# Kernel tuning notes

Measured on AMD Instinct MI355X. Metric: run time of the kernel, lower is better.

Reference implementation:

```python
import jax, jax.numpy as jnp
from jax import lax
import numpy as np

B, S, V, E, H, W = 32, 1024, 32000, 512, 512, 128  # batch, seq, vocab, emb, hidden, n_word_segments


def setup_inputs() -> dict:
    key = jax.random.key(0)
    ks = jax.random.split(key, 12)
    bound = 1.0 / np.sqrt(H)  # torch GRU default init: U(-1/sqrt(H), 1/sqrt(H))
    u = lambda k, shape: jax.random.uniform(k, shape, jnp.float32, -bound, bound)
    step = S // W
    inp = {
        "input_seqs": jax.random.randint(ks[0], (B, S), 0, V, dtype=jnp.int32),
        "input_lens": jnp.full((B,), S, dtype=jnp.int32),  # full lengths -> pack/pad is identity
        "hidden": jnp.zeros((2, B, H), jnp.float32),  # torch code ignores the passed hidden
        "layout": jnp.broadcast_to(jnp.arange(W + 1, dtype=jnp.int32) * step, (B, W + 1)),
        "emb": jax.random.normal(ks[1], (V, E), jnp.float32),
        "W_ih_f": u(ks[2], (3 * H, E)),
        "W_hh_f": u(ks[3], (3 * H, H)),
        "b_ih_f": u(ks[4], (3 * H,)),
        "b_hh_f": u(ks[5], (3 * H,)),
        "W_ih_b": u(ks[6], (3 * H, E)),
        "W_hh_b": u(ks[7], (3 * H, H)),
        "b_ih_b": u(ks[8], (3 * H,)),
        "b_hh_b": u(ks[9], (3 * H,)),
    }
    return inp


def _gru_dir(x, W_ih, W_hh, b_ih, b_hh, reverse):
    # x: [B,S,E]. Precompute input gates once (big GEMM), then scan the recurrence.
    gx = jnp.einsum('bse,ge->sbg', x, W_ih) + b_ih  # [S,B,3H], time-major
    h0 = jnp.zeros((x.shape[0], H), x.dtype)

    def step(h, g):
        gh = h @ W_hh.T + b_hh  # [B,3H]
        r = jax.nn.sigmoid(g[:, :H] + gh[:, :H])
        z = jax.nn.sigmoid(g[:, H:2 * H] + gh[:, H:2 * H])
        n = jnp.tanh(g[:, 2 * H:] + r * gh[:, 2 * H:])
        hn = (1.0 - z) * n + z * h
        return hn, hn

    hT, ys = lax.scan(step, h0, gx, reverse=reverse)  # ys: [S,B,H] aligned to original time order
    return ys.transpose(1, 0, 2), hT


def _segment_max(outputs, layout):
    # outputs: [B,S,2H]; layout: [B,W+1] sorted boundaries, layout[:,0]=0, layout[:,-1]=S.
    t = jnp.arange(S)
    seg = jax.vmap(lambda lay: jnp.searchsorted(lay, t, side='right') - 1)(layout)  # [B,S]
    gid = (jnp.arange(B)[:, None] * W + seg).reshape(-1)  # [B*S]
    flat = outputs.reshape(B * S, -1)
    mx = jax.ops.segment_max(flat, gid, num_segments=B * W)
    cnt = jax.ops.segment_sum(jnp.ones((B * S,), flat.dtype), gid, num_segments=B * W)
    mx = jnp.where(cnt[:, None] > 0, mx, 0.0)  # zero-pad empty segments (matches torch padding)
    return mx.reshape(B, W, -1)


def reference(input_seqs, input_lens, hidden, layout,
              emb, W_ih_f, W_hh_f, b_ih_f, b_hh_f, W_ih_b, W_hh_b, b_ih_b, b_hh_b):
    emb0 = emb.at[0].set(0.0)  # padding_idx=0
    x = emb0[input_seqs]  # [B,S,E]
    out_f, h_f = _gru_dir(x, W_ih_f, W_hh_f, b_ih_f, b_hh_f, reverse=False)
    out_b, h_b = _gru_dir(x, W_ih_b, W_hh_b, b_ih_b, b_hh_b, reverse=True)
    outputs = jnp.concatenate([out_f, out_b], axis=-1)  # [B,S,2H]
    hidden_out = jnp.stack([h_f, h_b], axis=0)  # [2,B,H]
    maxed = _segment_max(outputs, layout)  # [B,W,2H]
    return maxed, hidden_out
```

## Files before the change

### kernel.cpp

```cpp
#include <hip/hip_runtime.h>
#include <hip/hip_bf16.h>

#define Bb 32
#define Ss 1024
#define Vv 32000
#define Ee 512
#define Hh 512
#define Ww 128
#define GXC 3072
#define MR  (Bb * Ss)

typedef short short8  __attribute__((ext_vector_type(8)));
typedef float floatx4 __attribute__((ext_vector_type(4)));
typedef _Float16 f16x2 __attribute__((ext_vector_type(2)));
typedef unsigned long long u64;

__device__ inline float dot2f(unsigned w, unsigned h, float acc) {
  return __builtin_amdgcn_fdot2(__builtin_bit_cast(f16x2, w),
                                __builtin_bit_cast(f16x2, h), acc, false);
}
__device__ inline unsigned short bf16bits(float x) {
  return __builtin_bit_cast(unsigned short, __float2bfloat16(x));
}

template<typename T> __device__ inline T gxstore(float v);
template<> __device__ inline float gxstore<float>(float v) { return v; }
template<> __device__ inline __hip_bfloat16 gxstore<__hip_bfloat16>(float v) { return __float2bfloat16(v); }
template<typename T> __device__ inline float gxload(T v);
template<> __device__ inline float gxload<float>(float v) { return v; }
template<> __device__ inline float gxload<__hip_bfloat16>(__hip_bfloat16 v) { return __bfloat162float(v); }


__global__ void prep_emb(const float* __restrict__ emb, unsigned short* __restrict__ out) {
  int i = (blockIdx.x * 256 + threadIdx.x) * 4;
  float4 v = *reinterpret_cast<const float4*>(emb + i);
  bool z = (i < Ee);
  ushort4 o;
  o.x = z ? (unsigned short)0 : bf16bits(v.x);
  o.y = z ? (unsigned short)0 : bf16bits(v.y);
  o.z = z ? (unsigned short)0 : bf16bits(v.z);
  o.w = z ? (unsigned short)0 : bf16bits(v.w);
  *reinterpret_cast<ushort4*>(out + i) = o;
}

__global__ void prep_wih(const float* __restrict__ wf, const float* __restrict__ wb,
                         unsigned short* __restrict__ out) {
  int i = (blockIdx.x * 256 + threadIdx.x) * 4;
  const float* src = (i < 1536 * 512) ? (wf + i) : (wb + (i - 1536 * 512));
  float4 v = *reinterpret_cast<const float4*>(src);
  ushort4 o;
  o.x = bf16bits(v.x); o.y = bf16bits(v.y); o.z = bf16bits(v.z); o.w = bf16bits(v.w);
  *reinterpret_cast<ushort4*>(out + i) = o;
}

__global__ void prep_whh(const float* __restrict__ wf, const float* __restrict__ wb,
                         unsigned* __restrict__ out) {
  int o = blockIdx.x * 256 + threadIdx.x;
  int m    = o & 3;
  int u4   = o >> 2;
  int tid  = u4 & 511;
  int rest = u4 >> 9;
  int i    = rest & 15;
  int rest2 = rest >> 4;
  int g    = rest2 % 3;
  int rest3 = rest2 / 3;
  int j    = rest3 & 3;
  int dir  = rest3 >> 2;
  int c    = tid >> 2;
  int q    = tid & 3;
  int row  = g * 512 + j * 128 + c;
  int kp   = q * 64 + i * 4 + m;
  const float* W = dir ? wb : wf;
  unsigned lo = __builtin_bit_cast(unsigned short, (_Float16)W[(size_t)row * Hh + 2 * kp]);
  unsigned hi = __builtin_bit_cast(unsigned short, (_Float16)W[(size_t)row * Hh + 2 * kp + 1]);
  out[o] = lo | (hi << 16);
}

__global__ void zero_hx(unsigned* __restrict__ hxw) {
  hxw[blockIdx.x * 256 + threadIdx.x] = 0u;
}

template<typename GXT>
__global__ __launch_bounds__(256)
void gx_gemm(const int* __restrict__ seq, const unsigned short* __restrict__ embb,
             const unsigned short* __restrict__ wihb, GXT* __restrict__ gx) {
  __shared__ short As[128][80];
  __shared__ short Bs[128][80];
  __shared__ int toks[128];
  const int tid = threadIdx.x;
  const int m0 = blockIdx.y * 128;
  const int n0 = blockIdx.x * 128;
  if (tid < 128) {
    int r = m0 + tid;
    toks[tid] = seq[(r & 31) * Ss + (r >> 5)];
  }
  __syncthreads();
  const int lane = tid & 63, wave = tid >> 6;
  const int wm = (wave >> 1) * 64, wn = (wave & 1) * 64;
  floatx4 zero = {0.f, 0.f, 0.f, 0.f};
  floatx4 acc[4][4];
  #pragma unroll
  for (int a = 0; a < 4; ++a)
    #pragma unroll
    for (int c = 0; c < 4; ++c) acc[a][c] = zero;

  for (int k0 = 0; k0 < Ee; k0 += 64) {
    #pragma unroll
    for (int i = 0; i < 4; ++i) {
      int slot = i * 256 + tid;
      int row = slot >> 3, cq = (slot & 7) * 8;
      uint4 va = *reinterpret_cast<const uint4*>(embb + (size_t)toks[row] * Ee + k0 + cq);
      *reinterpret_cast<uint4*>(&As[row][cq]) = va;
      uint4 vb = *reinterpret_cast<const uint4*>(wihb + (size_t)(n0 + row) * Ee + k0 + cq);
      *reinterpret_cast<uint4*>(&Bs[row][cq]) = vb;
    }
    __syncthreads();
    #pragma unroll
    for (int ks = 0; ks < 2; ++ks) {
      short8 af[4], bfr[4];
      #pragma unroll
      for (int mi = 0; mi < 4; ++mi)
        af[mi] = *reinterpret_cast<const short8*>(&As[wm + mi * 16 + (lane & 15)][ks * 32 + (lane >> 4) * 8]);
      #pragma unroll
      for (int ni = 0; ni < 4; ++ni)
        bfr[ni] = *reinterpret_cast<const short8*>(&Bs[wn + ni * 16 + (lane & 15)][ks * 32 + (lane >> 4) * 8]);
      #pragma unroll
      for (int mi = 0; mi < 4; ++mi)
        #pragma unroll
        for (int ni = 0; ni < 4; ++ni)
          acc[mi][ni] = __builtin_amdgcn_mfma_f32_16x16x32_bf16(af[mi], bfr[ni], acc[mi][ni], 0, 0, 0);
    }
    __syncthreads();
  }
  #pragma unroll
  for (int mi = 0; mi < 4; ++mi) {
    #pragma unroll
    for (int ni = 0; ni < 4; ++ni) {
      int r0 = m0 + wm + mi * 16 + ((lane >> 4) * 4);
      int c  = n0 + wn + ni * 16 + (lane & 15);
      #pragma unroll
      for (int j = 0; j < 4; ++j)
        gx[(size_t)(r0 + j) * GXC + c] = gxstore<GXT>(acc[mi][ni][j]);
    }
  }
}


#define H16(M) M(0) M(1) M(2) M(3) M(4) M(5) M(6) M(7) \
               M(8) M(9) M(10) M(11) M(12) M(13) M(14) M(15)

#define WDECL(i) uint4 W0_##i, W1_##i, W2_##i;
#define WLOAD(i) W0_##i = wq[(i) * 512]; \
                 W1_##i = wq[(16 + (i)) * 512]; \
                 W2_##i = wq[(32 + (i)) * 512];
#define WPIN(i) asm volatile("" : "+v"(W0_##i.x), "+v"(W0_##i.y), "+v"(W0_##i.z), "+v"(W0_##i.w), \
                                  "+v"(W1_##i.x), "+v"(W1_##i.y), "+v"(W1_##i.z), "+v"(W1_##i.w), \
                                  "+v"(W2_##i.x), "+v"(W2_##i.y), "+v"(W2_##i.z), "+v"(W2_##i.w));
#define CHUNK(i) { uint4 Hq = hq4[i]; \
  s0 = dot2f(W0_##i.x, Hq.x, s0); s0 = dot2f(W0_##i.y, Hq.y, s0); \
  s0 = dot2f(W0_##i.z, Hq.z, s0); s0 = dot2f(W0_##i.w, Hq.w, s0); \
  s1 = dot2f(W1_##i.x, Hq.x, s1); s1 = dot2f(W1_##i.y, Hq.y, s1); \
  s1 = dot2f(W1_##i.z, Hq.z, s1); s1 = dot2f(W1_##i.w, Hq.w, s1); \
  s2 = dot2f(W2_##i.x, Hq.x, s2); s2 = dot2f(W2_##i.y, Hq.y, s2); \
  s2 = dot2f(W2_##i.z, Hq.z, s2); s2 = dot2f(W2_##i.w, Hq.w, s2); }

#define TAGOK1(a, want) \
  (((((unsigned)((a) >> 16)) & 0xffffu) == (want)) & \
   ((((unsigned)((a) >> 48))) == (want)))

template<typename GXT>
__global__ __launch_bounds__(512, 2)
void rnn_kernel(const GXT* __restrict__ gx, const unsigned* __restrict__ whh2,
                const float* __restrict__ bih_f, const float* __restrict__ bhh_f,
                const float* __restrict__ bih_b, const float* __restrict__ bhh_b,
                const int* __restrict__ layout, float* __restrict__ out,
                unsigned* __restrict__ hx) {
  __shared__ unsigned hbufw[544];
  __shared__ int lay[Ww + 1];
  const int tid   = threadIdx.x;
  const int j     = blockIdx.x >> 6;
  const int chain = blockIdx.x & 63;
  const int dir   = chain >> 5;
  const int b     = chain & 31;
  const int c     = tid >> 2;
  const int q     = tid & 3;
  const int col   = j * 128 + c;

  const uint4* wq = reinterpret_cast<const uint4*>(whh2)
                    + (size_t)(dir * 4 + j) * 48 * 512 + tid;
  H16(WDECL)
  H16(WLOAD)
  H16(WPIN)

  float bi0 = 0.f, bi1 = 0.f, bi2 = 0.f, bh0 = 0.f, bh1 = 0.f, bh2 = 0.f;
  if (q == 0) {
    const float* bi = dir ? bih_b : bih_f;
    const float* bh = dir ? bhh_b : bhh_f;
    bi0 = bi[col]; bi1 = bi[512 + col]; bi2 = bi[1024 + col];
    bh0 = bh[col]; bh1 = bh[512 + col]; bh2 = bh[1024 + col];
  }
  if (tid <= Ww) lay[tid] = layout[b * (Ww + 1) + tid];
  hbufw[tid] = 0u;
  if (tid < 32) hbufw[512 + tid] = 0u;
  __syncthreads();

  float h = 0.f, mx = -3.0e38f;
  int t = dir ? (Ss - 1) : 0;
  const int tstep = dir ? -1 : 1;
  int seg = dir ? (Ww - 1) : 0;
  int p = 0;

  float gr = 0.f, gz = 0.f, gn = 0.f;
  if (q == 0) {
    const GXT* gp = gx + (size_t)(t * Bb + b) * GXC + dir * 1536 + col;
    gr = gxload<GXT>(gp[0]); gz = gxload<GXT>(gp[512]); gn = gxload<GXT>(gp[1024]);
  }

  #pragma unroll 1
  for (int it = 0; it < Ss; ++it, t += tstep) {
    float ngr = 0.f, ngz = 0.f, ngn = 0.f;
    if (q == 0 && it + 1 < Ss) {
      const GXT* gp = gx + (size_t)((t + tstep) * Bb + b) * GXC + dir * 1536 + col;
      ngr = gxload<GXT>(gp[0]); ngz = gxload<GXT>(gp[512]); ngn = gxload<GXT>(gp[1024]);
    }
    float s0 = 0.f, s1 = 0.f, s2 = 0.f;
    const uint4* hq4 = reinterpret_cast<const uint4*>(hbufw) + p * 68 + q * 17;
    H16(CHUNK)
    H16(WPIN)
    { float u;
      u = __shfl_xor(s0, 1); s0 += u; u = __shfl_xor(s0, 2); s0 += u;
      u = __shfl_xor(s1, 1); s1 += u; u = __shfl_xor(s1, 2); s1 += u;
      u = __shfl_xor(s2, 1); s2 += u; u = __shfl_xor(s2, 2); s2 += u; }
    const int P = p ^ 1;
    if (q == 0) {
      float rs = gr + bi0 + bh0 + s0;
      float zs = gz + bi1 + bh1 + s1;
      float nh = bh2 + s2;
      float r = 1.f / (1.f + __expf(-rs));
      float z = 1.f / (1.f + __expf(-zs));
      float x = gn + bi2 + r * nh;
      x = fminf(fmaxf(x, -15.f), 15.f);
      float e = __expf(2.f * x);
      float n = (e - 1.f) / (e + 1.f);
      h = (1.f - z) * n + z * h;
      unsigned hb16 = (unsigned)__builtin_bit_cast(unsigned short, (_Float16)h);
      __hip_atomic_store(hx + ((((size_t)P * 64 + chain) * 4 + j) << 7) + c,
                         (((unsigned)(it + 1)) << 16) | hb16,
                         __ATOMIC_RELAXED, __HIP_MEMORY_SCOPE_AGENT);
      mx = fmaxf(mx, h);
      reinterpret_cast<_Float16*>(hbufw)[((P * 272 + j * 68 + (c >> 1)) << 1) | (c & 1)]
          = (_Float16)h;
      bool flush = dir ? (t == lay[seg]) : (t + 1 == lay[seg + 1]);
      if (flush) {
        out[(size_t)(b * Ww + seg) * 1024 + dir * 512 + col] = mx;
        mx = -3.0e38f;
        seg += tstep;
      }
    }
    if (it + 1 < Ss && tid < 192) {
      int s = tid >> 6, qd = tid & 63;
      int sib = s + (s >= j);
      const u64* src = reinterpret_cast<const u64*>(
          hx + ((((size_t)P * 64 + chain) * 4 + sib) << 7) + (qd << 1));
      const unsigned want = (unsigned)(it + 1);
      u64 a;
      for (;;) {
        a = __hip_atomic_load(src, __ATOMIC_RELAXED, __HIP_MEMORY_SCOPE_AGENT);
        if (TAGOK1(a, want)) break;
      }
      hbufw[P * 272 + sib * 68 + qd] =
          ((unsigned)a & 0xffffu) | (((unsigned)(a >> 32) & 0xffffu) << 16);
    }
    __syncthreads();
    p = P;
    gr = ngr; gz = ngz; gn = ngn;
  }
  if (q == 0)
    out[(size_t)Bb * Ww * 1024 + (size_t)dir * (Bb * Hh) + b * Hh + col] = h;
}

extern "C" void kernel_launch(void* const* d_in, const int* in_sizes, int n_in,
                              void* d_out, int out_size, void* d_ws, size_t ws_size,
                              hipStream_t stream) {
  const int*   seq    = (const int*)  d_in[0];
  const int*   layout = (const int*)  d_in[3];
  const float* emb    = (const float*)d_in[4];
  const float* Wih_f  = (const float*)d_in[5];
  const float* Whh_f  = (const float*)d_in[6];
  const float* bih_f  = (const float*)d_in[7];
  const float* bhh_f  = (const float*)d_in[8];
  const float* Wih_b  = (const float*)d_in[9];
  const float* Whh_b  = (const float*)d_in[10];
  const float* bih_b  = (const float*)d_in[11];
  const float* bhh_b  = (const float*)d_in[12];
  float* out = (float*)d_out;

  char* ws = (char*)d_ws;
  unsigned short* embb  = (unsigned short*)ws;
  unsigned short* wihb  = (unsigned short*)(ws + 32768000);
  unsigned*       whh2  = (unsigned*)      (ws + 35913728);
  unsigned*       hxw   = (unsigned*)      (ws + 39059456);
  void*           gxp   = (void*)          (ws + 39321600);

  const size_t need_f32 = 39321600ULL + (size_t)MR * GXC * 4;
  const size_t need_b16 = 39321600ULL + (size_t)MR * GXC * 2;
  if (ws_size < need_b16) return;

  prep_emb<<<(Vv * Ee) / 4 / 256, 256, 0, stream>>>(emb, embb);
  prep_wih<<<(GXC * Ee) / 4 / 256, 256, 0, stream>>>(Wih_f, Wih_b, wihb);
  prep_whh<<<(2 * 4 * 48 * 512 * 4) / 256, 256, 0, stream>>>(Whh_f, Whh_b, whh2);
  zero_hx<<<256, 256, 0, stream>>>(hxw);

  if (ws_size >= need_f32) {
    gx_gemm<float><<<dim3(GXC / 128, MR / 128), 256, 0, stream>>>(seq, embb, wihb, (float*)gxp);
    rnn_kernel<float><<<256, 512, 0, stream>>>((const float*)gxp, whh2,
                                               bih_f, bhh_f, bih_b, bhh_b, layout, out, hxw);
  } else {
    gx_gemm<__hip_bfloat16><<<dim3(GXC / 128, MR / 128), 256, 0, stream>>>(seq, embb, wihb, (__hip_bfloat16*)gxp);
    rnn_kernel<__hip_bfloat16><<<256, 512, 0, stream>>>((const __hip_bfloat16*)gxp, whh2,
                                                        bih_f, bhh_f, bih_b, bhh_b, layout, out, hxw);
  }
}
```

Baseline: 2.492 ms.

## Use MFMA 16x16x32 f16 for recurrent matvec with AGPR-resident weights

Replaces the per-thread fdot2 recurrent matvec with MFMA instructions. The hidden vector is fed as the A operand, so only one of the 16 rows is useful, and the W_hh slices stay pinned in accumulator registers. The W_hh prepack layout is reworked to match the MFMA B-operand layout. Gate sums go through a shared buffer, which adds an extra __syncthreads per timestep. The per-step latency is traded against wasting fifteen-sixteenths of the MFMA work and adding a barrier.

```diff
diff --git a/kernel.cpp b/kernel.cpp
--- a/kernel.cpp
+++ b/kernel.cpp
@@ -12,15 +12,14 @@
 
 typedef short short8  __attribute__((ext_vector_type(8)));
 typedef float floatx4 __attribute__((ext_vector_type(4)));
-typedef _Float16 f16x2 __attribute__((ext_vector_type(2)));
+typedef _Float16 f16x8 __attribute__((ext_vector_type(8)));
 typedef unsigned long long u64;
 
-__device__ inline float dot2f(unsigned w, unsigned h, float acc) {
-  return __builtin_amdgcn_fdot2(__builtin_bit_cast(f16x2, w),
-                                __builtin_bit_cast(f16x2, h), acc, false);
-}
 __device__ inline unsigned short bf16bits(float x) {
   return __builtin_bit_cast(unsigned short, __float2bfloat16(x));
+}
+__device__ inline unsigned f16w(float x) {
+  return (unsigned)__builtin_bit_cast(unsigned short, (_Float16)x);
 }
 
 template<typename T> __device__ inline T gxstore(float v);
@@ -56,24 +55,24 @@
 __global__ void prep_whh(const float* __restrict__ wf, const float* __restrict__ wb,
                          unsigned* __restrict__ out) {
   int o = blockIdx.x * 256 + threadIdx.x;
-  int m    = o & 3;
+  int d    = o & 3;
   int u4   = o >> 2;
-  int tid  = u4 & 511;
-  int rest = u4 >> 9;
-  int i    = rest & 15;
-  int rest2 = rest >> 4;
-  int g    = rest2 % 3;
-  int rest3 = rest2 / 3;
-  int j    = rest3 & 3;
-  int dir  = rest3 >> 2;
-  int c    = tid >> 2;
-  int q    = tid & 3;
-  int row  = g * 512 + j * 128 + c;
-  int kp   = q * 64 + i * 4 + m;
+  int l    = u4 & 63;
+  int kt   = (u4 >> 6) & 15;
+  int rest = u4 >> 10;
+  int s    = rest % 3;
+  int wj   = rest / 3;
+  int w    = wj & 7;
+  int dj   = wj >> 3;
+  int j    = dj & 3;
+  int dir  = dj >> 2;
+  int pair = w * 3 + s;
+  int g    = pair >> 3;
+  int n    = pair & 7;
+  int row  = g * 512 + j * 128 + n * 16 + (l & 15);
+  int k    = kt * 32 + ((l >> 4) << 3) + 2 * d;
   const float* W = dir ? wb : wf;
-  unsigned lo = __builtin_bit_cast(unsigned short, (_Float16)W[(size_t)row * Hh + 2 * kp]);
-  unsigned hi = __builtin_bit_cast(unsigned short, (_Float16)W[(size_t)row * Hh + 2 * kp + 1]);
-  out[o] = lo | (hi << 16);
+  out[o] = f16w(W[(size_t)row * Hh + k]) | (f16w(W[(size_t)row * Hh + k + 1]) << 16);
 }
 
 __global__ void zero_hx(unsigned* __restrict__ hxw) {
@@ -150,19 +149,20 @@
                M(8) M(9) M(10) M(11) M(12) M(13) M(14) M(15)
 
 #define WDECL(i) uint4 W0_##i, W1_##i, W2_##i;
-#define WLOAD(i) W0_##i = wq[(i) * 512]; \
-                 W1_##i = wq[(16 + (i)) * 512]; \
-                 W2_##i = wq[(32 + (i)) * 512];
-#define WPIN(i) asm volatile("" : "+v"(W0_##i.x), "+v"(W0_##i.y), "+v"(W0_##i.z), "+v"(W0_##i.w), \
-                                  "+v"(W1_##i.x), "+v"(W1_##i.y), "+v"(W1_##i.z), "+v"(W1_##i.w), \
-                                  "+v"(W2_##i.x), "+v"(W2_##i.y), "+v"(W2_##i.z), "+v"(W2_##i.w));
-#define CHUNK(i) { uint4 Hq = hq4[i]; \
-  s0 = dot2f(W0_##i.x, Hq.x, s0); s0 = dot2f(W0_##i.y, Hq.y, s0); \
-  s0 = dot2f(W0_##i.z, Hq.z, s0); s0 = dot2f(W0_##i.w, Hq.w, s0); \
-  s1 = dot2f(W1_##i.x, Hq.x, s1); s1 = dot2f(W1_##i.y, Hq.y, s1); \
-  s1 = dot2f(W1_##i.z, Hq.z, s1); s1 = dot2f(W1_##i.w, Hq.w, s1); \
-  s2 = dot2f(W2_##i.x, Hq.x, s2); s2 = dot2f(W2_##i.y, Hq.y, s2); \
-  s2 = dot2f(W2_##i.z, Hq.z, s2); s2 = dot2f(W2_##i.w, Hq.w, s2); }
+#define WLOAD(i) W0_##i = wq[(i) * 64]; \
+                 W1_##i = wq[(16 + (i)) * 64]; \
+                 W2_##i = wq[(32 + (i)) * 64];
+#define WPINA(i) asm volatile("" : "+a"(W0_##i.x), "+a"(W0_##i.y), "+a"(W0_##i.z), "+a"(W0_##i.w), \
+                                   "+a"(W1_##i.x), "+a"(W1_##i.y), "+a"(W1_##i.z), "+a"(W1_##i.w), \
+                                   "+a"(W2_##i.x), "+a"(W2_##i.y), "+a"(W2_##i.z), "+a"(W2_##i.w));
+#define CHUNKM(i) { \
+  short8 ar = *reinterpret_cast<const short8*>(hbytes + pb + ((i) << 6) + aoff); \
+  acc0 = __builtin_amdgcn_mfma_f32_16x16x32_f16(__builtin_bit_cast(f16x8, ar), \
+         __builtin_bit_cast(f16x8, W0_##i), acc0, 0, 0, 0); \
+  acc1 = __builtin_amdgcn_mfma_f32_16x16x32_f16(__builtin_bit_cast(f16x8, ar), \
+         __builtin_bit_cast(f16x8, W1_##i), acc1, 0, 0, 0); \
+  acc2 = __builtin_amdgcn_mfma_f32_16x16x32_f16(__builtin_bit_cast(f16x8, ar), \
+         __builtin_bit_cast(f16x8, W2_##i), acc2, 0, 0, 0); }
 
 #define TAGOK1(a, want) \
   (((((unsigned)((a) >> 16)) & 0xffffu) == (want)) & \
@@ -175,33 +175,35 @@
                 const float* __restrict__ bih_b, const float* __restrict__ bhh_b,
                 const int* __restrict__ layout, float* __restrict__ out,
                 unsigned* __restrict__ hx) {
-  __shared__ unsigned hbufw[544];
+  __shared__ unsigned hbufw[512];
+  __shared__ float sbuf[3][128];
   __shared__ int lay[Ww + 1];
   const int tid   = threadIdx.x;
+  const int w     = tid >> 6;
+  const int lane  = tid & 63;
   const int j     = blockIdx.x >> 6;
   const int chain = blockIdx.x & 63;
   const int dir   = chain >> 5;
   const int b     = chain & 31;
-  const int c     = tid >> 2;
-  const int q     = tid & 3;
-  const int col   = j * 128 + c;
 
   const uint4* wq = reinterpret_cast<const uint4*>(whh2)
-                    + (size_t)(dir * 4 + j) * 48 * 512 + tid;
+                    + (size_t)((dir * 4 + j) * 8 + w) * 3072 + lane;
   H16(WDECL)
   H16(WLOAD)
-  H16(WPIN)
-
-  float bi0 = 0.f, bi1 = 0.f, bi2 = 0.f, bh0 = 0.f, bh1 = 0.f, bh2 = 0.f;
-  if (q == 0) {
+  H16(WPINA)
+
+  float br0 = 0.f, bz0 = 0.f, bi2 = 0.f, bh2 = 0.f;
+  if (tid < 128) {
     const float* bi = dir ? bih_b : bih_f;
-    const float* bh = dir ? bhh_b : bhh_f;
-    bi0 = bi[col]; bi1 = bi[512 + col]; bi2 = bi[1024 + col];
-    bh0 = bh[col]; bh1 = bh[512 + col]; bh2 = bh[1024 + col];
+    const float* bv = dir ? bhh_b : bhh_f;
+    int col = j * 128 + tid;
+    br0 = bi[col] + bv[col];
+    bz0 = bi[512 + col] + bv[512 + col];
+    bi2 = bi[1024 + col];
+    bh2 = bv[1024 + col];
   }
   if (tid <= Ww) lay[tid] = layout[b * (Ww + 1) + tid];
   hbufw[tid] = 0u;
-  if (tid < 32) hbufw[512 + tid] = 0u;
   __syncthreads();
 
   float h = 0.f, mx = -3.0e38f;
@@ -209,33 +211,39 @@
   const int tstep = dir ? -1 : 1;
   int seg = dir ? (Ww - 1) : 0;
   int p = 0;
+  const char* hbytes = reinterpret_cast<const char*>(hbufw);
+  const int aoff = (lane >> 4) << 4;
 
   float gr = 0.f, gz = 0.f, gn = 0.f;
-  if (q == 0) {
-    const GXT* gp = gx + (size_t)(t * Bb + b) * GXC + dir * 1536 + col;
+  if (tid < 128) {
+    const GXT* gp = gx + (size_t)(t * Bb + b) * GXC + dir * 1536 + j * 128 + tid;
     gr = gxload<GXT>(gp[0]); gz = gxload<GXT>(gp[512]); gn = gxload<GXT>(gp[1024]);
   }
 
   #pragma unroll 1
   for (int it = 0; it < Ss; ++it, t += tstep) {
     float ngr = 0.f, ngz = 0.f, ngn = 0.f;
-    if (q == 0 && it + 1 < Ss) {
-      const GXT* gp = gx + (size_t)((t + tstep) * Bb + b) * GXC + dir * 1536 + col;
+    if (tid < 128 && it + 1 < Ss) {
+      const GXT* gp = gx + (size_t)((t + tstep) * Bb + b) * GXC + dir * 1536 + j * 128 + tid;
       ngr = gxload<GXT>(gp[0]); ngz = gxload<GXT>(gp[512]); ngn = gxload<GXT>(gp[1024]);
     }
-    float s0 = 0.f, s1 = 0.f, s2 = 0.f;
-    const uint4* hq4 = reinterpret_cast<const uint4*>(hbufw) + p * 68 + q * 17;
-    H16(CHUNK)
-    H16(WPIN)
-    { float u;
-      u = __shfl_xor(s0, 1); s0 += u; u = __shfl_xor(s0, 2); s0 += u;
-      u = __shfl_xor(s1, 1); s1 += u; u = __shfl_xor(s1, 2); s1 += u;
-      u = __shfl_xor(s2, 1); s2 += u; u = __shfl_xor(s2, 2); s2 += u; }
+    floatx4 acc0 = {0.f, 0.f, 0.f, 0.f};
+    floatx4 acc1 = acc0, acc2 = acc0;
+    const int pb = p << 10;
+    H16(CHUNKM)
+    H16(WPINA)
+    if (lane < 16) {
+      int p0 = w * 3;
+      sbuf[p0 >> 3][((p0 & 7) << 4) + lane]             = acc0[0];
+      sbuf[(p0 + 1) >> 3][(((p0 + 1) & 7) << 4) + lane] = acc1[0];
+      sbuf[(p0 + 2) >> 3][(((p0 + 2) & 7) << 4) + lane] = acc2[0];
+    }
+    __syncthreads();
     const int P = p ^ 1;
-    if (q == 0) {
-      float rs = gr + bi0 + bh0 + s0;
-      float zs = gz + bi1 + bh1 + s1;
-      float nh = bh2 + s2;
+    if (tid < 128) {
+      float rs = gr + br0 + sbuf[0][tid];
+      float zs = gz + bz0 + sbuf[1][tid];
+      float nh = bh2 + sbuf[2][tid];
       float r = 1.f / (1.f + __expf(-rs));
       float z = 1.f / (1.f + __expf(-zs));
       float x = gn + bi2 + r * nh;
@@ -244,22 +252,21 @@
       float n = (e - 1.f) / (e + 1.f);
       h = (1.f - z) * n + z * h;
       unsigned hb16 = (unsigned)__builtin_bit_cast(unsigned short, (_Float16)h);
-      __hip_atomic_store(hx + ((((size_t)P * 64 + chain) * 4 + j) << 7) + c,
+      __hip_atomic_store(hx + ((((size_t)P * 64 + chain) * 4 + j) << 7) + tid,
                          (((unsigned)(it + 1)) << 16) | hb16,
                          __ATOMIC_RELAXED, __HIP_MEMORY_SCOPE_AGENT);
       mx = fmaxf(mx, h);
-      reinterpret_cast<_Float16*>(hbufw)[((P * 272 + j * 68 + (c >> 1)) << 1) | (c & 1)]
-          = (_Float16)h;
+      reinterpret_cast<_Float16*>(hbufw)[P * 512 + j * 128 + tid] = (_Float16)h;
       bool flush = dir ? (t == lay[seg]) : (t + 1 == lay[seg + 1]);
       if (flush) {
-        out[(size_t)(b * Ww + seg) * 1024 + dir * 512 + col] = mx;
+        out[(size_t)(b * Ww + seg) * 1024 + dir * 512 + j * 128 + tid] = mx;
         mx = -3.0e38f;
         seg += tstep;
       }
     }
     if (it + 1 < Ss && tid < 192) {
-      int s = tid >> 6, qd = tid & 63;
-      int sib = s + (s >= j);
+      int s2 = tid >> 6, qd = tid & 63;
+      int sib = s2 + (s2 >= j);
       const u64* src = reinterpret_cast<const u64*>(
           hx + ((((size_t)P * 64 + chain) * 4 + sib) << 7) + (qd << 1));
       const unsigned want = (unsigned)(it + 1);
@@ -268,15 +275,15 @@
         a = __hip_atomic_load(src, __ATOMIC_RELAXED, __HIP_MEMORY_SCOPE_AGENT);
         if (TAGOK1(a, want)) break;
       }
-      hbufw[P * 272 + sib * 68 + qd] =
+      hbufw[P * 256 + sib * 64 + qd] =
           ((unsigned)a & 0xffffu) | (((unsigned)(a >> 32) & 0xffffu) << 16);
     }
     __syncthreads();
     p = P;
     gr = ngr; gz = ngz; gn = ngn;
   }
-  if (q == 0)
-    out[(size_t)Bb * Ww * 1024 + (size_t)dir * (Bb * Hh) + b * Hh + col] = h;
+  if (tid < 128)
+    out[(size_t)Bb * Ww * 1024 + (size_t)dir * (Bb * Hh) + (size_t)b * Hh + j * 128 + tid] = h;
 }
 
 extern "C" void kernel_launch(void* const* d_in, const int* in_sizes, int n_in,
@@ -308,7 +315,7 @@
 
   prep_emb<<<(Vv * Ee) / 4 / 256, 256, 0, stream>>>(emb, embb);
   prep_wih<<<(GXC * Ee) / 4 / 256, 256, 0, stream>>>(Wih_f, Wih_b, wihb);
-  prep_whh<<<(2 * 4 * 48 * 512 * 4) / 256, 256, 0, stream>>>(Whh_f, Whh_b, whh2);
+  prep_whh<<<786432 / 256, 256, 0, stream>>>(Whh_f, Whh_b, whh2);
   zero_hx<<<256, 256, 0, stream>>>(hxw);
 
   if (ws_size >= need_f32) {
```

New measurement: 3.165 ms. 1.27x slower.
